# Performance work log

Measured on AMD Instinct MI355X. Metric: run time of the kernel, lower is better.

## Reference

```python
import jax, jax.numpy as jnp
import numpy as np

IN_FEATURES = 4096
OUT_FEATURES = 16384
BATCH = 4
SEQ = 2048


def setup_inputs() -> dict:
    key = jax.random.key(0)
    kx, kw, ks = jax.random.split(key, 3)
    x = jax.random.normal(kx, (BATCH, SEQ, IN_FEATURES), dtype=jnp.float32)
    # int8-quantized weight values in [-127, 127]
    weight = jax.random.randint(kw, (OUT_FEATURES, IN_FEATURES), -127, 128, dtype=jnp.int32).astype(jnp.int8)
    # per-output-row dequant scale (positive, small, like |w|_max/127)
    scale = (jax.random.uniform(ks, (OUT_FEATURES, 1), dtype=jnp.float32) * 0.02 + 1e-4)
    return {"x": x, "weight": weight, "scale": scale}


def reference(x, weight, scale):
    # float_weight = weight.float() * scale  -> [out, in]
    float_weight = weight.astype(jnp.float32) * scale
    # F.linear(x, W) = x @ W.T  (no bias)
    return jnp.einsum('bsi,oi->bso', x, float_weight)
```

## Files before the change

### kernel.cpp

```cpp
#include <hip/hip_runtime.h>
#include <hip/hip_bf16.h>
#include <stdint.h>

#define M_TOTAL 8192
#define K_TOTAL 4096
#define N_TOTAL 16384
#define BM 256
#define BN 256
#define KT 64
#define TILE_B 16384
#define BUF_S 32768
#define NBUF 4

typedef int i32x4 __attribute__((ext_vector_type(4)));

static __device__ __forceinline__ void async16(const void* g, void* l) {
    __builtin_amdgcn_global_load_lds((const __attribute__((address_space(1))) unsigned int*)g,
                                     (__attribute__((address_space(3))) unsigned int*)l,
                                     16, 0, 0);
}


__global__ __launch_bounds__(256) void cvt_x_fused(const float* __restrict__ x,
                                                   char* __restrict__ xq,
                                                   float* __restrict__ sx) {
    int r = blockIdx.x * 4 + (threadIdx.x >> 6);
    int l = threadIdx.x & 63;
    const float4* p = reinterpret_cast<const float4*>(x + (size_t)r * K_TOTAL) + l;
    float4 v[16];
    float m = 0.f;
    #pragma unroll
    for (int i = 0; i < 16; ++i) {
        v[i] = p[i * 64];
        m = fmaxf(m, fmaxf(fmaxf(fabsf(v[i].x), fabsf(v[i].y)), fmaxf(fabsf(v[i].z), fabsf(v[i].w))));
    }
    #pragma unroll
    for (int off = 32; off; off >>= 1) m = fmaxf(m, __shfl_xor(m, off, 64));
    m = fmaxf(m, 1e-20f);
    if (l == 0) sx[r] = m / 127.f;
    float inv = 127.f / m;

    char* base = xq + (size_t)(r >> 8) * (KT * TILE_B)
               + ((r >> 4) & 15) * 1024
               + (((r & 15) | (((l >> 2) & 3) << 4)) * 16)
               + ((l & 3) << 2)
               + ((l >> 4) * 16384);
    #pragma unroll
    for (int i = 0; i < 16; ++i) {
        int q0 = (int)__builtin_rintf(v[i].x * inv);
        int q1 = (int)__builtin_rintf(v[i].y * inv);
        int q2 = (int)__builtin_rintf(v[i].z * inv);
        int q3 = (int)__builtin_rintf(v[i].w * inv);
        int wv = (q0 & 0xff) | ((q1 & 0xff) << 8) | ((q2 & 0xff) << 16) | (q3 << 24);
        *reinterpret_cast<int*>(base + (size_t)i * 4 * 16384) = wv;
    }
}

__global__ __launch_bounds__(256) void cvt_w_pack(const int* __restrict__ w,
                                                  char* __restrict__ wq) {
    size_t j = (size_t)blockIdx.x * 256 + threadIdx.x;
    int nt = (int)(j >> 16);
    int j2 = (int)(j & 65535);
    int kt = j2 >> 10;
    int f  = (j2 >> 6) & 15;
    int l  = j2 & 63;
    int r  = nt * 256 + f * 16 + (l & 15);
    int k0 = kt * 64 + ((l >> 4) << 4);
    const int4* s = reinterpret_cast<const int4*>(w + (size_t)r * K_TOTAL + k0);
    int4 v0 = s[0], v1 = s[1], v2 = s[2], v3 = s[3];
    int4 d;
    d.x = (v0.x&0xff) | ((v0.y&0xff)<<8) | ((v0.z&0xff)<<16) | (v0.w<<24);
    d.y = (v1.x&0xff) | ((v1.y&0xff)<<8) | ((v1.z&0xff)<<16) | (v1.w<<24);
    d.z = (v2.x&0xff) | ((v2.y&0xff)<<8) | ((v2.z&0xff)<<16) | (v2.w<<24);
    d.w = (v3.x&0xff) | ((v3.y&0xff)<<8) | ((v3.z&0xff)<<16) | (v3.w<<24);
    *reinterpret_cast<int4*>(wq + j * 16) = d;
}


#define BAR()    { asm volatile("" ::: "memory"); __builtin_amdgcn_s_barrier(); asm volatile("" ::: "memory"); }
#define VMC4()   asm volatile("s_waitcnt vmcnt(4)" ::: "memory")
#define VMC0()   asm volatile("s_waitcnt vmcnt(0)" ::: "memory")
#define PRIO1()  __builtin_amdgcn_s_setprio(1)
#define PRIO0()  __builtin_amdgcn_s_setprio(0)
#define SCHEDB() __builtin_amdgcn_sched_barrier(0)

#define STG(ts, so) { \
    async16(aS + (size_t)(ts)*TILE_B + tid*16,        ldsc + (so) + tid*16); \
    async16(aS + (size_t)(ts)*TILE_B + 8192 + tid*16, ldsc + (so) + 8192 + tid*16); \
    async16(bS + (size_t)(ts)*TILE_B + tid*16,        ldsc + (so) + 16384 + tid*16); \
    async16(bS + (size_t)(ts)*TILE_B + 8192 + tid*16, ldsc + (so) + 24576 + tid*16); }

#define RDF0(bo) { \
    _Pragma("unroll") for (int ni = 0; ni < 4; ++ni) bfr0[ni] = *(const i32x4*)(bRd + (bo) + ni * 1024); \
    _Pragma("unroll") for (int mi = 0; mi < 8; ++mi) afr0[mi] = *(const i32x4*)(aRd + (bo) + mi * 1024); }

#define RDF1(bo) { \
    _Pragma("unroll") for (int ni = 0; ni < 4; ++ni) bfr1[ni] = *(const i32x4*)(bRd + (bo) + ni * 1024); \
    _Pragma("unroll") for (int mi = 0; mi < 8; ++mi) afr1[mi] = *(const i32x4*)(aRd + (bo) + mi * 1024); }

#define MMA0() { PRIO1(); \
    _Pragma("unroll") for (int mi = 0; mi < 8; ++mi) { _Pragma("unroll") \
        for (int ni = 0; ni < 4; ++ni) \
            acc[mi][ni] = __builtin_amdgcn_mfma_i32_16x16x64_i8(afr0[mi], bfr0[ni], acc[mi][ni], 0, 0, 0); } \
    PRIO0(); }

#define MMA1() { PRIO1(); \
    _Pragma("unroll") for (int mi = 0; mi < 8; ++mi) { _Pragma("unroll") \
        for (int ni = 0; ni < 4; ++ni) \
            acc[mi][ni] = __builtin_amdgcn_mfma_i32_16x16x64_i8(afr1[mi], bfr1[ni], acc[mi][ni], 0, 0, 0); } \
    PRIO0(); }

#define WIN(st, sb, rb, RDFx, MMAx) { \
    STG(st, sb); \
    RDFx(rb); \
    SCHEDB(); \
    MMAx(); \
    SCHEDB(); \
    VMC4(); BAR(); }

__global__ __launch_bounds__(512, 2) void gemm_kernel(const char* __restrict__ A,
                                                      const char* __restrict__ B,
                                                      const float* __restrict__ scale,
                                                      const float* __restrict__ sx,
                                                      float* __restrict__ out) {
    extern __shared__ char ldsc[];
    const int tid  = threadIdx.x;
    const int lane = tid & 63;
    const int wave = tid >> 6;
    const int wm = wave >> 2;
    const int wn = wave & 3;

    int orig = blockIdx.x;
    int swzid = (orig & 7) * 256 + (orig >> 3);
    int mt = swzid & 31;
    int nt = swzid >> 5;

    const char* aS = A + (size_t)mt * (KT * TILE_B);
    const char* bS = B + (size_t)nt * (KT * TILE_B);

    const char* aRd = ldsc + wm * 8192 + lane * 16;
    const char* bRd = ldsc + 16384 + wn * 4096 + lane * 16;

    i32x4 acc[8][4];
    #pragma unroll
    for (int mi = 0; mi < 8; ++mi)
        #pragma unroll
        for (int ni = 0; ni < 4; ++ni)
            acc[mi][ni] = (i32x4){0, 0, 0, 0};

    i32x4 afr0[8], bfr0[4], afr1[8], bfr1[4];

    STG(0, 0); STG(1, BUF_S); STG(2, 2 * BUF_S);
    VMC4();
    BAR();
    RDF0(0);

    for (int T = 0; T < 60; T += 4) {
        WIN(T + 3, 3 * BUF_S, 1 * BUF_S, RDF1, MMA0);
        WIN(T + 4, 0,         2 * BUF_S, RDF0, MMA1);
        WIN(T + 5, 1 * BUF_S, 3 * BUF_S, RDF1, MMA0);
        WIN(T + 6, 2 * BUF_S, 0,         RDF0, MMA1);
    }
    WIN(63, 3 * BUF_S, 1 * BUF_S, RDF1, MMA0);
    RDF0(2 * BUF_S);
    SCHEDB();
    MMA1();
    SCHEDB();
    VMC0(); BAR();
    RDF1(3 * BUF_S);
    SCHEDB();
    MMA0();
    SCHEDB();
    MMA1();

    int m0 = mt * BM, n0 = nt * BN;
    int col0 = n0 + wn * 64 + (lane & 15);
    int row0 = m0 + wm * 128 + ((lane >> 4) << 2);
    float swv[4];
    #pragma unroll
    for (int ni = 0; ni < 4; ++ni) swv[ni] = scale[col0 + ni * 16];
    #pragma unroll
    for (int mi = 0; mi < 8; ++mi) {
        #pragma unroll
        for (int j = 0; j < 4; ++j) {
            int r = row0 + mi * 16 + j;
            float sr = sx[r];
            #pragma unroll
            for (int ni = 0; ni < 4; ++ni) {
                out[(size_t)r * N_TOTAL + (col0 + ni * 16)] = (float)acc[mi][ni][j] * sr * swv[ni];
            }
        }
    }
}


__global__ __launch_bounds__(256) void naive_kernel(const float* __restrict__ x, const int* __restrict__ w,
                                                    const float* __restrict__ scale, float* __restrict__ out) {
    int n = blockIdx.x * 256 + threadIdx.x;
    int m = blockIdx.y;
    const float* xr = x + (size_t)m * K_TOTAL;
    const int*   wr = w + (size_t)n * K_TOTAL;
    float acc = 0.f;
    for (int k = 0; k < K_TOTAL; k += 4) {
        float4 xv = *(const float4*)(xr + k);
        int4   wv = *(const int4*)(wr + k);
        acc += xv.x * (float)wv.x + xv.y * (float)wv.y + xv.z * (float)wv.z + xv.w * (float)wv.w;
    }
    out[(size_t)m * N_TOTAL + n] = acc * scale[n];
}

extern "C" void kernel_launch(void* const* d_in, const int* in_sizes, int n_in,
                              void* d_out, int out_size, void* d_ws, size_t ws_size,
                              hipStream_t stream) {
    const float* x     = (const float*)d_in[0];
    const int*   w     = (const int*)d_in[1];
    const float* scale = (const float*)d_in[2];
    float* out = (float*)d_out;

    const size_t xq_bytes = (size_t)M_TOTAL * K_TOTAL;
    const size_t wq_bytes = (size_t)N_TOTAL * K_TOTAL;
    const size_t sx_bytes = (size_t)M_TOTAL * 4;

    if (ws_size >= xq_bytes + wq_bytes + sx_bytes) {
        char*  xq = (char*)d_ws;
        char*  wq = (char*)d_ws + xq_bytes;
        float* sx = (float*)((char*)d_ws + xq_bytes + wq_bytes);
        (void)hipFuncSetAttribute((const void*)gemm_kernel,
                                  hipFuncAttributeMaxDynamicSharedMemorySize, NBUF * BUF_S);
        cvt_x_fused<<<M_TOTAL / 4, 256, 0, stream>>>(x, xq, sx);
        cvt_w_pack<<<(N_TOTAL / 256) * (K_TOTAL / 16), 256, 0, stream>>>(w, wq);
        gemm_kernel<<<(M_TOTAL / BM) * (N_TOTAL / BN), 512, NBUF * BUF_S, stream>>>(xq, wq, scale, sx, out);
    } else {
        dim3 g(N_TOTAL / 256, M_TOTAL);
        naive_kernel<<<g, 256, 0, stream>>>(x, w, scale, out);
    }
}
```

Measured before the change: 739.1 us.

## Switch int8 GEMM to 32x32x32 MFMA with matching operand packing

Replaces the 16x16x64 int8 MFMA tiles with 32x32x32 int8 MFMA tiles. The pre-pack kernels for x and w are reworked to emit the fragment layout the larger instruction expects, split into two K halves per 64-wide tile. The LDS read offsets and the epilogue row/column mapping are changed to match. The larger instruction is meant to need fewer MFMA issues and LDS fragment reads per unit of work, but the epilogue now reads sx per element and the store pattern changes.

```diff
diff --git a/kernel.cpp b/kernel.cpp
--- a/kernel.cpp
+++ b/kernel.cpp
@@ -12,7 +12,8 @@
 #define BUF_S 32768
 #define NBUF 4
 
-typedef int i32x4 __attribute__((ext_vector_type(4)));
+typedef int i32x4  __attribute__((ext_vector_type(4)));
+typedef int i32x16 __attribute__((ext_vector_type(16)));
 
 static __device__ __forceinline__ void async16(const void* g, void* l) {
     __builtin_amdgcn_global_load_lds((const __attribute__((address_space(1))) unsigned int*)g,
@@ -41,10 +42,11 @@
     float inv = 127.f / m;
 
     char* base = xq + (size_t)(r >> 8) * (KT * TILE_B)
-               + ((r >> 4) & 15) * 1024
-               + (((r & 15) | (((l >> 2) & 3) << 4)) * 16)
-               + ((l & 3) << 2)
-               + ((l >> 4) * 16384);
+               + ((l >> 4) * 16384)
+               + (((l >> 3) & 1) * 8192)
+               + (((r >> 5) & 7) * 1024)
+               + (((r & 31) | (((l >> 2) & 1) << 5)) * 16)
+               + ((l & 3) << 2);
     #pragma unroll
     for (int i = 0; i < 16; ++i) {
         int q0 = (int)__builtin_rintf(v[i].x * inv);
@@ -62,10 +64,11 @@
     int nt = (int)(j >> 16);
     int j2 = (int)(j & 65535);
     int kt = j2 >> 10;
-    int f  = (j2 >> 6) & 15;
+    int ks = (j2 >> 9) & 1;
+    int f  = (j2 >> 6) & 7;
     int l  = j2 & 63;
-    int r  = nt * 256 + f * 16 + (l & 15);
-    int k0 = kt * 64 + ((l >> 4) << 4);
+    int r  = nt * 256 + f * 32 + (l & 31);
+    int k0 = kt * 64 + ks * 32 + ((l >> 5) << 4);
     const int4* s = reinterpret_cast<const int4*>(w + (size_t)r * K_TOTAL + k0);
     int4 v0 = s[0], v1 = s[1], v2 = s[2], v3 = s[3];
     int4 d;
@@ -91,23 +94,31 @@
     async16(bS + (size_t)(ts)*TILE_B + 8192 + tid*16, ldsc + (so) + 24576 + tid*16); }
 
 #define RDF0(bo) { \
-    _Pragma("unroll") for (int ni = 0; ni < 4; ++ni) bfr0[ni] = *(const i32x4*)(bRd + (bo) + ni * 1024); \
-    _Pragma("unroll") for (int mi = 0; mi < 8; ++mi) afr0[mi] = *(const i32x4*)(aRd + (bo) + mi * 1024); }
+    _Pragma("unroll") for (int ks = 0; ks < 2; ++ks) { \
+        _Pragma("unroll") for (int ni = 0; ni < 2; ++ni) \
+            bfr0[ks*2+ni] = *(const i32x4*)(bRd + (bo) + ks*8192 + ni*1024); \
+        _Pragma("unroll") for (int mi = 0; mi < 4; ++mi) \
+            afr0[ks*4+mi] = *(const i32x4*)(aRd + (bo) + ks*8192 + mi*1024); } }
 
 #define RDF1(bo) { \
-    _Pragma("unroll") for (int ni = 0; ni < 4; ++ni) bfr1[ni] = *(const i32x4*)(bRd + (bo) + ni * 1024); \
-    _Pragma("unroll") for (int mi = 0; mi < 8; ++mi) afr1[mi] = *(const i32x4*)(aRd + (bo) + mi * 1024); }
+    _Pragma("unroll") for (int ks = 0; ks < 2; ++ks) { \
+        _Pragma("unroll") for (int ni = 0; ni < 2; ++ni) \
+            bfr1[ks*2+ni] = *(const i32x4*)(bRd + (bo) + ks*8192 + ni*1024); \
+        _Pragma("unroll") for (int mi = 0; mi < 4; ++mi) \
+            afr1[ks*4+mi] = *(const i32x4*)(aRd + (bo) + ks*8192 + mi*1024); } }
 
 #define MMA0() { PRIO1(); \
-    _Pragma("unroll") for (int mi = 0; mi < 8; ++mi) { _Pragma("unroll") \
-        for (int ni = 0; ni < 4; ++ni) \
-            acc[mi][ni] = __builtin_amdgcn_mfma_i32_16x16x64_i8(afr0[mi], bfr0[ni], acc[mi][ni], 0, 0, 0); } \
+    _Pragma("unroll") for (int ks = 0; ks < 2; ++ks) { \
+        _Pragma("unroll") for (int mi = 0; mi < 4; ++mi) { _Pragma("unroll") \
+            for (int ni = 0; ni < 2; ++ni) \
+                acc[mi][ni] = __builtin_amdgcn_mfma_i32_32x32x32_i8(afr0[ks*4+mi], bfr0[ks*2+ni], acc[mi][ni], 0, 0, 0); } } \
     PRIO0(); }
 
 #define MMA1() { PRIO1(); \
-    _Pragma("unroll") for (int mi = 0; mi < 8; ++mi) { _Pragma("unroll") \
-        for (int ni = 0; ni < 4; ++ni) \
-            acc[mi][ni] = __builtin_amdgcn_mfma_i32_16x16x64_i8(afr1[mi], bfr1[ni], acc[mi][ni], 0, 0, 0); } \
+    _Pragma("unroll") for (int ks = 0; ks < 2; ++ks) { \
+        _Pragma("unroll") for (int mi = 0; mi < 4; ++mi) { _Pragma("unroll") \
+            for (int ni = 0; ni < 2; ++ni) \
+                acc[mi][ni] = __builtin_amdgcn_mfma_i32_32x32x32_i8(afr1[ks*4+mi], bfr1[ks*2+ni], acc[mi][ni], 0, 0, 0); } } \
     PRIO0(); }
 
 #define WIN(st, sb, rb, RDFx, MMAx) { \
@@ -138,15 +149,15 @@
     const char* aS = A + (size_t)mt * (KT * TILE_B);
     const char* bS = B + (size_t)nt * (KT * TILE_B);
 
-    const char* aRd = ldsc + wm * 8192 + lane * 16;
-    const char* bRd = ldsc + 16384 + wn * 4096 + lane * 16;
-
-    i32x4 acc[8][4];
-    #pragma unroll
-    for (int mi = 0; mi < 8; ++mi)
+    const char* aRd = ldsc + wm * 4096 + lane * 16;
+    const char* bRd = ldsc + 16384 + wn * 2048 + lane * 16;
+
+    i32x16 acc[4][2];
+    #pragma unroll
+    for (int mi = 0; mi < 4; ++mi)
         #pragma unroll
-        for (int ni = 0; ni < 4; ++ni)
-            acc[mi][ni] = (i32x4){0, 0, 0, 0};
+        for (int ni = 0; ni < 2; ++ni)
+            acc[mi][ni] = (i32x16)(0);
 
     i32x4 afr0[8], bfr0[4], afr1[8], bfr1[4];
 
@@ -174,20 +185,17 @@
     MMA1();
 
     int m0 = mt * BM, n0 = nt * BN;
-    int col0 = n0 + wn * 64 + (lane & 15);
-    int row0 = m0 + wm * 128 + ((lane >> 4) << 2);
-    float swv[4];
-    #pragma unroll
-    for (int ni = 0; ni < 4; ++ni) swv[ni] = scale[col0 + ni * 16];
-    #pragma unroll
-    for (int mi = 0; mi < 8; ++mi) {
+    int col0 = n0 + wn * 64 + (lane & 31);
+    int rbase = m0 + wm * 128 + ((lane >> 5) << 2);
+    #pragma unroll
+    for (int ni = 0; ni < 2; ++ni) {
+        float sw_ = scale[col0 + ni * 32];
         #pragma unroll
-        for (int j = 0; j < 4; ++j) {
-            int r = row0 + mi * 16 + j;
-            float sr = sx[r];
+        for (int mi = 0; mi < 4; ++mi) {
             #pragma unroll
-            for (int ni = 0; ni < 4; ++ni) {
-                out[(size_t)r * N_TOTAL + (col0 + ni * 16)] = (float)acc[mi][ni][j] * sr * swv[ni];
+            for (int reg = 0; reg < 16; ++reg) {
+                int r = rbase + mi * 32 + (reg & 3) + 8 * (reg >> 2);
+                out[(size_t)r * N_TOTAL + (col0 + ni * 32)] = (float)acc[mi][ni][reg] * sx[r] * sw_;
             }
         }
     }
```

Result: slower. 794.8 us (+7.5%).

## Restructure GEMM pipeline to two-tile double-buffered stages with full waits

Applied to the files above, without the earlier changes.

Replaces the 4-buffer rolling pipeline (one K-tile per window, partial vmcnt(4) wait, fragment prefetch across windows) with a scheme that processes two K-tiles per stage and loads the next two tiles into the other buffer pair. Barriers are halved, but each stage now waits for all outstanding loads (vmcnt(0)), and LDS fragment reads are no longer overlapped with the previous MMA. This trades finer-grained overlap for fewer synchronisation points.

```diff
diff --git a/kernel.cpp b/kernel.cpp
--- a/kernel.cpp
+++ b/kernel.cpp
@@ -78,7 +78,6 @@
 
 
 #define BAR()    { asm volatile("" ::: "memory"); __builtin_amdgcn_s_barrier(); asm volatile("" ::: "memory"); }
-#define VMC4()   asm volatile("s_waitcnt vmcnt(4)" ::: "memory")
 #define VMC0()   asm volatile("s_waitcnt vmcnt(0)" ::: "memory")
 #define PRIO1()  __builtin_amdgcn_s_setprio(1)
 #define PRIO0()  __builtin_amdgcn_s_setprio(0)
@@ -109,14 +108,6 @@
         for (int ni = 0; ni < 4; ++ni) \
             acc[mi][ni] = __builtin_amdgcn_mfma_i32_16x16x64_i8(afr1[mi], bfr1[ni], acc[mi][ni], 0, 0, 0); } \
     PRIO0(); }
-
-#define WIN(st, sb, rb, RDFx, MMAx) { \
-    STG(st, sb); \
-    RDFx(rb); \
-    SCHEDB(); \
-    MMAx(); \
-    SCHEDB(); \
-    VMC4(); BAR(); }
 
 __global__ __launch_bounds__(512, 2) void gemm_kernel(const char* __restrict__ A,
                                                       const char* __restrict__ B,
@@ -150,28 +141,33 @@
 
     i32x4 afr0[8], bfr0[4], afr1[8], bfr1[4];
 
-    STG(0, 0); STG(1, BUF_S); STG(2, 2 * BUF_S);
-    VMC4();
+    STG(0, 0); STG(1, BUF_S);
+    VMC0();
     BAR();
-    RDF0(0);
-
-    for (int T = 0; T < 60; T += 4) {
-        WIN(T + 3, 3 * BUF_S, 1 * BUF_S, RDF1, MMA0);
-        WIN(T + 4, 0,         2 * BUF_S, RDF0, MMA1);
-        WIN(T + 5, 1 * BUF_S, 3 * BUF_S, RDF1, MMA0);
-        WIN(T + 6, 2 * BUF_S, 0,         RDF0, MMA1);
-    }
-    WIN(63, 3 * BUF_S, 1 * BUF_S, RDF1, MMA0);
-    RDF0(2 * BUF_S);
+
+    for (int w = 0; w < 30; w += 2) {
+        STG(2 * w + 2, 2 * BUF_S); STG(2 * w + 3, 3 * BUF_S);
+        RDF0(0); RDF1(BUF_S);
+        SCHEDB();
+        MMA0(); MMA1();
+        SCHEDB();
+        VMC0(); BAR();
+        STG(2 * w + 4, 0); STG(2 * w + 5, BUF_S);
+        RDF0(2 * BUF_S); RDF1(3 * BUF_S);
+        SCHEDB();
+        MMA0(); MMA1();
+        SCHEDB();
+        VMC0(); BAR();
+    }
+    STG(62, 2 * BUF_S); STG(63, 3 * BUF_S);
+    RDF0(0); RDF1(BUF_S);
     SCHEDB();
-    MMA1();
+    MMA0(); MMA1();
     SCHEDB();
     VMC0(); BAR();
-    RDF1(3 * BUF_S);
+    RDF0(2 * BUF_S); RDF1(3 * BUF_S);
     SCHEDB();
-    MMA0();
-    SCHEDB();
-    MMA1();
+    MMA0(); MMA1();
 
     int m0 = mt * BM, n0 = nt * BN;
     int col0 = n0 + wn * 64 + (lane & 15);
```

After: 772.4 us. +4.5%, slower.
